# Optimization experiments

Measured on AMD Instinct MI355X. Metric: run time of the kernel, lower is better.

## Reference

```python
import jax, jax.numpy as jnp
import numpy as np

TAU = 2.0      # spikingjelly MultiStepLIFNode default tau
VTH = 1.0      # default v_threshold
ALPHA = 4.0    # default Sigmoid surrogate alpha
EPS = 1e-5     # BatchNorm eps

# --- STE sign for binarized conv weights (Binarize.apply, det mode, scale=1) ---
@jax.custom_vjp
def ste_sign(x):
    return jnp.sign(x)

def _ss_fwd(x):
    return jnp.sign(x), None

def _ss_bwd(_, g):
    return (g,)

ste_sign.defvjp(_ss_fwd, _ss_bwd)

# --- Heaviside spike with sigmoid surrogate gradient ---
@jax.custom_vjp
def spike_fn(x):
    return (x >= 0.0).astype(x.dtype)

def _sp_fwd(x):
    return (x >= 0.0).astype(x.dtype), x

def _sp_bwd(x, g):
    s = jax.nn.sigmoid(ALPHA * x)
    return (g * ALPHA * s * (1.0 - s),)

spike_fn.defvjp(_sp_fwd, _sp_bwd)

def lif(x):
    # x: [T,B,C,H,W]; LIF with v_reset=None (soft reset), decay_input=True,
    # detach_reset=True (stop_gradient on the reset term).
    def step(v, xt):
        v = v + (xt - v) / TAU
        s = spike_fn(v - VTH)
        v = v - jax.lax.stop_gradient(s) * VTH
        return v, s
    v0 = jnp.zeros_like(x[0])
    _, spikes = jax.lax.scan(step, v0, x)
    return spikes

def conv3x3(x, w, groups=1):
    # x: [N,C,H,W], w: [O, C//groups, 3, 3], stride 1, pad 1
    return jax.lax.conv_general_dilated(
        x, w, window_strides=(1, 1), padding=((1, 1), (1, 1)),
        dimension_numbers=('NCHW', 'OIHW', 'NCHW'),
        feature_group_count=groups)

def setup_inputs() -> dict:
    key = jax.random.key(0)
    k1, k2, k3 = jax.random.split(key, 3)
    x = jax.random.normal(k1, (4, 8, 256, 64, 64), dtype=jnp.float32)
    w1 = jax.random.normal(k2, (192, 256, 3, 3), dtype=jnp.float32) * 0.05
    gamma = jnp.ones((192,), dtype=jnp.float32)
    beta = jnp.zeros((192,), dtype=jnp.float32)
    w2 = jax.random.normal(k3, (320, 48, 3, 3), dtype=jnp.float32) * 0.05
    return {'x': x, 'w1': w1, 'gamma': gamma, 'beta': beta, 'w2': w2}

def reference(x, w1, gamma, beta, w2):
    T, B, C, H, W = x.shape
    s = lif(x).reshape(T * B, C, H, W)          # spikes, flatten(0,1)
    y = conv3x3(s, w1)                          # conv1 (bias=False)
    # BatchNorm2d in training mode: batch stats over (N,H,W), biased var
    mean = y.mean(axis=(0, 2, 3))
    var = y.var(axis=(0, 2, 3))
    yb = (y - mean[None, :, None, None]) * jax.lax.rsqrt(var + EPS)[None, :, None, None]
    yb = yb * gamma[None, :, None, None] + beta[None, :, None, None]
    hidden = yb.shape[1]
    x1 = yb.reshape(T, B, hidden, H, W)
    z = conv3x3(yb, ste_sign(w2), groups=4)     # binarized-weight conv, groups=4
    x2 = z.reshape(T, B, -1, H, W)
    return jnp.concatenate((x1, x2), axis=2)    # [T,B,output_size,H,W]
```

## Files before the change

### kernel.cpp

```cpp
#include <hip/hip_runtime.h>

typedef __bf16 bf16x8 __attribute__((ext_vector_type(8)));
typedef float f32x4 __attribute__((ext_vector_type(4)));

#define DEV static __device__ __forceinline__

DEV ushort f2bf(float f) {
  unsigned u = __builtin_bit_cast(unsigned, f);
  u = (u + 0x7FFFu + ((u >> 16) & 1u)) >> 16;
  return (ushort)u;
}
DEV float bf2f(ushort h) {
  unsigned u = ((unsigned)h) << 16;
  return __builtin_bit_cast(float, u);
}
DEV void gll16(const void* g, void* l) {
  __builtin_amdgcn_global_load_lds((const __attribute__((address_space(1))) void*)g,
                                   (__attribute__((address_space(3))) void*)l, 16, 0, 0);
}

#define Y_OFF      71368704ull
#define WR1_OFF    121700352ull
#define WR2_OFF    122585088ull
#define STATS_OFF  122953728ull
#define ZERO_OFF   122955264ull
#define PART_OFF   122959360ull

DEV void border_px(int p, int& h, int& w) {
  if (p < 66)       { h = 0;       w = p; }
  else if (p < 132) { h = 65;      w = p - 66; }
  else if (p < 196) { h = p - 131; w = 0; }
  else              { h = p - 195; w = 65; }
}
__global__ void halo1_kernel(ushort* __restrict__ S) {
  const int idx = blockIdx.x * 256 + threadIdx.x;
  const int n = idx / 16640, r = idx % 16640;
  const int p = r >> 6, c4 = r & 63;
  int h, w; border_px(p, h, w);
  ushort4 z; z.x = 0; z.y = 0; z.z = 0; z.w = 0;
  *(ushort4*)&S[((size_t)((n * 66 + h) * 66 + w) << 8) + c4 * 4] = z;
}
__global__ void halo2_kernel(ushort* __restrict__ Yb) {
  const int idx = blockIdx.x * 256 + threadIdx.x;
  const int n = idx / 12480, r = idx % 12480;
  const int p = r / 48, c4 = r % 48;
  int h, w; border_px(p, h, w);
  ushort4 z; z.x = 0; z.y = 0; z.z = 0; z.w = 0;
  *(ushort4*)&Yb[(size_t)((n * 66 + h) * 66 + w) * 192 + c4 * 4] = z;
}

__global__ __launch_bounds__(256) void lif_kernel(const float* __restrict__ x,
                                                  ushort* __restrict__ S) {
  const int bi = blockIdx.x;
  const int jq = bi >> 9;
  const int b  = (bi >> 6) & 7;
  const int h  = bi & 63;
  const int tid = threadIdx.x;
  const int w0 = (tid & 15) << 2;
  const int cg = (tid >> 4) + (jq << 4);
  const int c0 = cg << 2;

  float v[4][4];
#pragma unroll
  for (int a = 0; a < 4; ++a)
#pragma unroll
    for (int k = 0; k < 4; ++k) v[a][k] = 0.f;

#pragma unroll
  for (int t = 0; t < 4; ++t) {
    const int n = t * 8 + b;
    ushort sp[4][4];
#pragma unroll
    for (int a = 0; a < 4; ++a) {
      const float4 xv = *(const float4*)(x + ((size_t)(n * 256 + c0 + a) << 12) + (h << 6) + w0);
      const float xa[4] = {xv.x, xv.y, xv.z, xv.w};
#pragma unroll
      for (int k = 0; k < 4; ++k) {
        v[a][k] += (xa[k] - v[a][k]) * 0.5f;
        const bool s = v[a][k] >= 1.0f;
        sp[a][k] = s ? (ushort)0x3F80 : (ushort)0;
        v[a][k] -= s ? 1.0f : 0.0f;
      }
    }
#pragma unroll
    for (int k = 0; k < 4; ++k) {
      ushort4 o4; o4.x = sp[0][k]; o4.y = sp[1][k]; o4.z = sp[2][k]; o4.w = sp[3][k];
      *(ushort4*)(S + ((size_t)((n * 66 + h + 1) * 66 + (w0 + k + 1)) << 8) + c0) = o4;
    }
  }
}

__global__ void prep_w1_kernel(const float* __restrict__ w1, ushort* __restrict__ Wr1) {
  const int idx = blockIdx.x * 256 + threadIdx.x;
  const int pos = idx / 49152, r = idx % 49152;
  const int o = r >> 8, c = r & 255;
  Wr1[idx] = f2bf(w1[(o * 256 + c) * 9 + pos]);
}
__global__ void prep_w2_kernel(const float* __restrict__ w2, ushort* __restrict__ Wr2) {
  const int idx = blockIdx.x * 256 + threadIdx.x;
  const int gp = idx / 5120, r = idx % 5120;
  const int o = r >> 6, c = r & 63;
  const int g = gp / 9, pos = gp % 9;
  float v = 0.f;
  if (c < 48) {
    const float wv = w2[((g * 80 + o) * 48 + c) * 9 + pos];
    v = (wv > 0.f) ? 1.f : ((wv < 0.f) ? -1.f : 0.f);
  }
  Wr2[idx] = f2bf(v);
}

__global__ __launch_bounds__(256) void conv1_kernel(const ushort* __restrict__ S,
                                                    const ushort* __restrict__ Wr1,
                                                    ushort* __restrict__ Y,
                                                    float* __restrict__ Pp) {
  __shared__ ushort ldsA[12288];
  __shared__ ushort ldsB[8192];
  const int tid = threadIdx.x;
  const int l = tid & 63, wv = tid >> 6;
  const int wrow = wv >> 1, wcol = wv & 1;
  const int col = l & 15, quad = l >> 4;
  const int bid = ((blockIdx.x & 7) << 7) | (blockIdx.x >> 3);
  const int pxb = bid << 7;
  const int n = pxb >> 12;
  const int h0 = (pxb >> 6) & 63;
  const int n66h0 = n * 66 + h0;

  int goA[6], loA[6];
#pragma unroll
  for (int ii = 0; ii < 6; ++ii) {
    const int s = ii * 256 + tid;
    const int kc = s / 768, r = s % 768;
    const int row = r >> 2, op = r & 3;
    const int ol = (op - (row >> 1)) & 3;
    goA[ii] = row * 256 + kc * 32 + ol * 8;
    loA[ii] = s * 8;
  }
  int hrB[4], wB_[4], cB[4], loB[4];
#pragma unroll
  for (int ii = 0; ii < 4; ++ii) {
    const int s = ii * 256 + tid;
    const int kc = s >> 9, r = s & 511;
    const int pxl = r >> 2, op = r & 3;
    const int ol = (op - (pxl >> 1)) & 3;
    hrB[ii] = pxl >> 6; wB_[ii] = pxl & 63;
    cB[ii] = kc * 32 + ol * 8;
    loB[ii] = s * 8;
  }
  int offA[6], offB[4];
#pragma unroll
  for (int i = 0; i < 6; ++i) {
    const int row = wrow * 96 + i * 16 + col;
    offA[i] = row * 32 + (((quad + (row >> 1)) & 3) << 3);
  }
#pragma unroll
  for (int j = 0; j < 4; ++j) {
    const int row = wcol * 64 + j * 16 + col;
    offB[j] = row * 32 + (((quad + (row >> 1)) & 3) << 3);
  }

  f32x4 acc[6][4];
#pragma unroll
  for (int i = 0; i < 6; ++i)
#pragma unroll
    for (int j = 0; j < 4; ++j) acc[i][j] = (f32x4){0.f, 0.f, 0.f, 0.f};

  for (int it = 0; it < 36; ++it) {
    const int pos = it >> 2, cc = it & 3;
    const int kh = pos / 3, kw = pos - 3 * kh;
    const int c0 = cc << 6;
    __syncthreads();
#pragma unroll
    for (int ii = 0; ii < 6; ++ii)
      gll16(Wr1 + pos * 49152 + c0 + goA[ii], &ldsA[loA[ii]]);
#pragma unroll
    for (int ii = 0; ii < 4; ++ii)
      gll16(S + ((n66h0 + hrB[ii] + kh) * 66 + wB_[ii] + kw) * 256 + c0 + cB[ii],
            &ldsB[loB[ii]]);
    __syncthreads();
#pragma unroll
    for (int kc = 0; kc < 2; ++kc) {
      bf16x8 bf[4];
#pragma unroll
      for (int j = 0; j < 4; ++j)
        bf[j] = *(const bf16x8*)&ldsB[kc * 4096 + offB[j]];
#pragma unroll
      for (int i = 0; i < 6; ++i) {
        const bf16x8 af = *(const bf16x8*)&ldsA[kc * 6144 + offA[i]];
#pragma unroll
        for (int j = 0; j < 4; ++j)
          acc[i][j] = __builtin_amdgcn_mfma_f32_16x16x32_bf16(af, bf[j], acc[i][j], 0, 0, 0);
      }
    }
  }
#pragma unroll
  for (int i = 0; i < 6; ++i) {
    const int o = wrow * 96 + i * 16 + quad * 4;
#pragma unroll
    for (int j = 0; j < 4; ++j) {
      const int px = pxb + wcol * 64 + j * 16 + col;
      ushort4 st;
      st.x = f2bf(acc[i][j].x); st.y = f2bf(acc[i][j].y);
      st.z = f2bf(acc[i][j].z); st.w = f2bf(acc[i][j].w);
      *(ushort4*)&Y[px * 192 + o] = st;
    }
  }
#pragma unroll
  for (int i = 0; i < 6; ++i) {
    float s[4], q[4];
#pragma unroll
    for (int k = 0; k < 4; ++k) { s[k] = 0.f; q[k] = 0.f; }
#pragma unroll
    for (int j = 0; j < 4; ++j)
#pragma unroll
      for (int k = 0; k < 4; ++k) {
        const float v = acc[i][j][k];
        s[k] += v; q[k] += v * v;
      }
#pragma unroll
    for (int m = 1; m < 16; m <<= 1)
#pragma unroll
      for (int k = 0; k < 4; ++k) {
        s[k] += __shfl_xor(s[k], m, 64);
        q[k] += __shfl_xor(q[k], m, 64);
      }
    if (col == 0) {
      const int oc = wrow * 96 + i * 16 + quad * 4;
      const int slot = (int)blockIdx.x * 2 + wcol;
#pragma unroll
      for (int k = 0; k < 4; ++k) {
        Pp[(oc + k) * 2048 + slot] = s[k];
        Pp[(192 + oc + k) * 2048 + slot] = q[k];
      }
    }
  }
}

__global__ void reduce_stats_kernel(const float* __restrict__ Pp, float* __restrict__ stats) {
  const int r = blockIdx.x, t = threadIdx.x;
  const float4 a = *(const float4*)&Pp[r * 2048 + t * 8];
  const float4 b = *(const float4*)&Pp[r * 2048 + t * 8 + 4];
  float s = a.x + a.y + a.z + a.w + b.x + b.y + b.z + b.w;
#pragma unroll
  for (int m = 32; m; m >>= 1) s += __shfl_xor(s, m, 64);
  __shared__ float ls[4];
  if ((t & 63) == 0) ls[t >> 6] = s;
  __syncthreads();
  if (t == 0) stats[r] = ls[0] + ls[1] + ls[2] + ls[3];
}

__global__ void bn_kernel(const ushort* __restrict__ Y, const float* __restrict__ stats,
                          const float* __restrict__ gamma, const float* __restrict__ beta,
                          float* __restrict__ out, ushort* __restrict__ Yb) {
  __shared__ float lds[13056];
  const int tid = threadIdx.x;
  const int n = blockIdx.x >> 6, h = blockIdx.x & 63;
  const int cq = tid % 48, wsub = tid / 48;
  const int c0 = cq * 4;
  float a[4], bb[4];
#pragma unroll
  for (int j = 0; j < 4; ++j) {
    const int c = c0 + j;
    const float mean = stats[c] * (1.f / 131072.f);
    const float var = stats[192 + c] * (1.f / 131072.f) - mean * mean;
    const float r = rsqrtf(var + 1e-5f);
    a[j] = gamma[c] * r;
    bb[j] = beta[c] - mean * a[j];
  }
  const int pxrow = n * 4096 + h * 64;
  for (int i = 0; i < 16; ++i) {
    const int w = i * 4 + wsub;
    const ushort4 yv = *(const ushort4*)&Y[(pxrow + w) * 192 + c0];
    float f[4];
    f[0] = a[0] * bf2f(yv.x) + bb[0];
    f[1] = a[1] * bf2f(yv.y) + bb[1];
    f[2] = a[2] * bf2f(yv.z) + bb[2];
    f[3] = a[3] * bf2f(yv.w) + bb[3];
    ushort4 ob;
    ob.x = f2bf(f[0]); ob.y = f2bf(f[1]); ob.z = f2bf(f[2]); ob.w = f2bf(f[3]);
    *(ushort4*)&Yb[(size_t)((n * 66 + h + 1) * 66 + (w + 1)) * 192 + c0] = ob;
#pragma unroll
    for (int j = 0; j < 4; ++j) lds[(c0 + j) * 68 + w] = f[j];
  }
  __syncthreads();
  const int w4 = (tid & 15) << 2, cz = tid >> 4;
  for (int i = 0; i < 16; ++i) {
    const int c = cz * 16 + i;
    const float4 v = *(const float4*)&lds[c * 68 + w4];
    *(float4*)&out[((size_t)(n * 512 + c) << 12) + h * 64 + w4] = v;
  }
}

__global__ __launch_bounds__(256) void conv2_kernel(const ushort* __restrict__ Yb,
                                                    const ushort* __restrict__ Wr2,
                                                    const ushort* __restrict__ zb,
                                                    float* __restrict__ out) {
  __shared__ ushort ldsA[16384];
  __shared__ ushort ldsB[6144];
  const int tid = threadIdx.x;
  const int l = tid & 63, wv = tid >> 6;
  const int col = l & 15, quad = l >> 4;
  const int g = blockIdx.y;
  const int g48 = g * 48;
  const int bid = ((blockIdx.x & 7) << 6) | (blockIdx.x >> 3);
  const int pxb = bid << 8;
  const int n = pxb >> 12;
  const int h0 = (pxb >> 6) & 63;
  const int n66h0 = n * 66 + h0;

  int hrA[8], wA[8], cA[8], vA[8], loA[8];
#pragma unroll
  for (int ii = 0; ii < 8; ++ii) {
    const int s = ii * 256 + tid;
    const int kc = s >> 10, r = s & 1023;
    const int pxl = r >> 2, op = r & 3;
    const int ol = (op - (pxl >> 1)) & 3;
    hrA[ii] = pxl >> 6; wA[ii] = pxl & 63;
    const int c = kc * 32 + ol * 8;
    cA[ii] = c; vA[ii] = (c < 48);
    loA[ii] = s * 8;
  }
  int gB[3], vB[3], loB[3];
#pragma unroll
  for (int ii = 0; ii < 3; ++ii) {
    const int s = ii * 256 + tid;
    const int kc = s / 384, r = s % 384;
    const int row = r >> 2, op = r & 3;
    const int ol = (op - (row >> 1)) & 3;
    vB[ii] = (row < 80);
    gB[ii] = row * 64 + kc * 32 + ol * 8;
    loB[ii] = s * 8;
  }
  int offA[4], offB[5];
#pragma unroll
  for (int i = 0; i < 4; ++i) {
    const int row = wv * 64 + i * 16 + col;
    offA[i] = row * 32 + (((quad + (row >> 1)) & 3) << 3);
  }
#pragma unroll
  for (int j = 0; j < 5; ++j) {
    const int row = j * 16 + col;
    offB[j] = row * 32 + (((quad + (row >> 1)) & 3) << 3);
  }

  f32x4 acc[4][5];
#pragma unroll
  for (int i = 0; i < 4; ++i)
#pragma unroll
    for (int j = 0; j < 5; ++j) acc[i][j] = (f32x4){0.f, 0.f, 0.f, 0.f};

  for (int pos = 0; pos < 9; ++pos) {
    const int kh = pos / 3, kw = pos - 3 * kh;
    const int wbase = (g * 9 + pos) * 5120;
    __syncthreads();
#pragma unroll
    for (int ii = 0; ii < 8; ++ii) {
      const ushort* p = vA[ii]
        ? Yb + (size_t)((n66h0 + hrA[ii] + kh) * 66 + wA[ii] + kw) * 192 + g48 + cA[ii]
        : zb;
      gll16(p, &ldsA[loA[ii]]);
    }
#pragma unroll
    for (int ii = 0; ii < 3; ++ii) {
      const ushort* p = vB[ii] ? Wr2 + wbase + gB[ii] : zb;
      gll16(p, &ldsB[loB[ii]]);
    }
    __syncthreads();
#pragma unroll
    for (int kc = 0; kc < 2; ++kc) {
      bf16x8 bw[5];
#pragma unroll
      for (int j = 0; j < 5; ++j)
        bw[j] = *(const bf16x8*)&ldsB[kc * 3072 + offB[j]];
#pragma unroll
      for (int i = 0; i < 4; ++i) {
        const bf16x8 af = *(const bf16x8*)&ldsA[kc * 8192 + offA[i]];
#pragma unroll
        for (int j = 0; j < 5; ++j)
          acc[i][j] = __builtin_amdgcn_mfma_f32_16x16x32_bf16(af, bw[j], acc[i][j], 0, 0, 0);
      }
    }
  }
#pragma unroll
  for (int i = 0; i < 4; ++i) {
    const int pxl = (pxb & 4095) + wv * 64 + i * 16 + quad * 4;
#pragma unroll
    for (int j = 0; j < 5; ++j) {
      const int o = 192 + g * 80 + j * 16 + col;
      float4 v4;
      v4.x = acc[i][j].x; v4.y = acc[i][j].y; v4.z = acc[i][j].z; v4.w = acc[i][j].w;
      *(float4*)&out[((size_t)(n * 512 + o) << 12) + pxl] = v4;
    }
  }
}

extern "C" void kernel_launch(void* const* d_in, const int* in_sizes, int n_in,
                              void* d_out, int out_size, void* d_ws, size_t ws_size,
                              hipStream_t stream) {
  const float* x     = (const float*)d_in[0];
  const float* w1    = (const float*)d_in[1];
  const float* gamma = (const float*)d_in[2];
  const float* beta  = (const float*)d_in[3];
  const float* w2    = (const float*)d_in[4];
  float* out = (float*)d_out;
  char* ws = (char*)d_ws;

  ushort* S   = (ushort*)ws;
  ushort* Yb  = (ushort*)ws;
  ushort* Y   = (ushort*)(ws + Y_OFF);
  ushort* Wr1 = (ushort*)(ws + WR1_OFF);
  ushort* Wr2 = (ushort*)(ws + WR2_OFF);
  float* stats = (float*)(ws + STATS_OFF);
  const ushort* zb = (const ushort*)(ws + ZERO_OFF);
  float* Pp = (float*)(ws + PART_OFF);

  hipMemsetAsync(ws + ZERO_OFF, 0, 4096, stream);
  hipLaunchKernelGGL(prep_w1_kernel, dim3(1728), dim3(256), 0, stream, w1, Wr1);
  hipLaunchKernelGGL(prep_w2_kernel, dim3(720), dim3(256), 0, stream, w2, Wr2);
  hipLaunchKernelGGL(halo1_kernel, dim3(2080), dim3(256), 0, stream, S);
  hipLaunchKernelGGL(lif_kernel, dim3(2048), dim3(256), 0, stream, x, S);
  hipLaunchKernelGGL(conv1_kernel, dim3(1024), dim3(256), 0, stream, S, Wr1, Y, Pp);
  hipLaunchKernelGGL(reduce_stats_kernel, dim3(384), dim3(256), 0, stream, Pp, stats);
  hipLaunchKernelGGL(halo2_kernel, dim3(1560), dim3(256), 0, stream, Yb);
  hipLaunchKernelGGL(bn_kernel, dim3(2048), dim3(192), 0, stream, Y, stats, gamma, beta, out, Yb);
  hipLaunchKernelGGL(conv2_kernel, dim3(512, 4), dim3(256), 0, stream, Yb, Wr2, zb, out);
}
```

Baseline: 714.4 us.

## Double-buffer LDS tiles in conv1 to overlap global loads with MFMA

Converts the conv1 K-loop to a two-stage ping-pong LDS pipeline: the next tile's global_load_lds is issued before computing the current tile, halving barriers per step. Also precomputes combined B-operand offsets to cut per-iteration address arithmetic. LDS usage doubles to roughly 80KB per block and launch bounds request two blocks per CU, which may constrain occupancy or registers.

```diff
diff --git a/kernel.cpp b/kernel.cpp
--- a/kernel.cpp
+++ b/kernel.cpp
@@ -109,12 +109,12 @@
   Wr2[idx] = f2bf(v);
 }
 
-__global__ __launch_bounds__(256) void conv1_kernel(const ushort* __restrict__ S,
-                                                    const ushort* __restrict__ Wr1,
-                                                    ushort* __restrict__ Y,
-                                                    float* __restrict__ Pp) {
-  __shared__ ushort ldsA[12288];
-  __shared__ ushort ldsB[8192];
+__global__ __launch_bounds__(256, 2) void conv1_kernel(const ushort* __restrict__ S,
+                                                       const ushort* __restrict__ Wr1,
+                                                       ushort* __restrict__ Y,
+                                                       float* __restrict__ Pp) {
+  __shared__ ushort ldsA[2][12288];
+  __shared__ ushort ldsB[2][8192];
   const int tid = threadIdx.x;
   const int l = tid & 63, wv = tid >> 6;
   const int wrow = wv >> 1, wcol = wv & 1;
@@ -135,15 +135,14 @@
     goA[ii] = row * 256 + kc * 32 + ol * 8;
     loA[ii] = s * 8;
   }
-  int hrB[4], wB_[4], cB[4], loB[4];
+  int goB[4], loB[4];
 #pragma unroll
   for (int ii = 0; ii < 4; ++ii) {
     const int s = ii * 256 + tid;
     const int kc = s >> 9, r = s & 511;
     const int pxl = r >> 2, op = r & 3;
     const int ol = (op - (pxl >> 1)) & 3;
-    hrB[ii] = pxl >> 6; wB_[ii] = pxl & 63;
-    cB[ii] = kc * 32 + ol * 8;
+    goB[ii] = ((pxl >> 6) * 66 + (pxl & 63)) * 256 + kc * 32 + ol * 8;
     loB[ii] = s * 8;
   }
   int offA[6], offB[4];
@@ -164,34 +163,48 @@
 #pragma unroll
     for (int j = 0; j < 4; ++j) acc[i][j] = (f32x4){0.f, 0.f, 0.f, 0.f};
 
-  for (int it = 0; it < 36; ++it) {
-    const int pos = it >> 2, cc = it & 3;
+  auto stage = [&](int it2, int buf) {
+    const int pos = it2 >> 2, cc = it2 & 3;
     const int kh = pos / 3, kw = pos - 3 * kh;
     const int c0 = cc << 6;
-    __syncthreads();
+    const int uA = pos * 49152 + c0;
+    const int uB = ((n66h0 + kh) * 66 + kw) * 256 + c0;
 #pragma unroll
     for (int ii = 0; ii < 6; ++ii)
-      gll16(Wr1 + pos * 49152 + c0 + goA[ii], &ldsA[loA[ii]]);
+      gll16(Wr1 + uA + goA[ii], &ldsA[buf][loA[ii]]);
 #pragma unroll
     for (int ii = 0; ii < 4; ++ii)
-      gll16(S + ((n66h0 + hrB[ii] + kh) * 66 + wB_[ii] + kw) * 256 + c0 + cB[ii],
-            &ldsB[loB[ii]]);
-    __syncthreads();
+      gll16(S + uB + goB[ii], &ldsB[buf][loB[ii]]);
+  };
+
+  auto computeTile = [&](int buf) {
 #pragma unroll
     for (int kc = 0; kc < 2; ++kc) {
       bf16x8 bf[4];
 #pragma unroll
       for (int j = 0; j < 4; ++j)
-        bf[j] = *(const bf16x8*)&ldsB[kc * 4096 + offB[j]];
+        bf[j] = *(const bf16x8*)&ldsB[buf][kc * 4096 + offB[j]];
 #pragma unroll
       for (int i = 0; i < 6; ++i) {
-        const bf16x8 af = *(const bf16x8*)&ldsA[kc * 6144 + offA[i]];
+        const bf16x8 af = *(const bf16x8*)&ldsA[buf][kc * 6144 + offA[i]];
 #pragma unroll
         for (int j = 0; j < 4; ++j)
           acc[i][j] = __builtin_amdgcn_mfma_f32_16x16x32_bf16(af, bf[j], acc[i][j], 0, 0, 0);
       }
     }
-  }
+  };
+
+  stage(0, 0);
+  __syncthreads();
+  for (int it = 0; it < 36; it += 2) {
+    stage(it + 1, 1);
+    computeTile(0);
+    __syncthreads();
+    if (it + 2 < 36) stage(it + 2, 0);
+    computeTile(1);
+    __syncthreads();
+  }
+
 #pragma unroll
   for (int i = 0; i < 6; ++i) {
     const int o = wrow * 96 + i * 16 + quad * 4;
```

Result: faster. 615.0 us (-13.9%).
